# Kernel optimization log

Measured on AMD Instinct MI355X. Metric: run time of the kernel, lower is better.

Reference implementation:

```python
import jax, jax.numpy as jnp
import numpy as np

NUM_HEADS = 32
NUM_KV_HEADS = 8
HEAD_DIM = 128
SCALE = 0.08838834764831845  # 1/sqrt(HEAD_DIM)
SEQ_LEN = 2048
NEG_INF = -1e30


def setup_inputs() -> dict:
    key = jax.random.key(0)
    k1, k2, k3 = jax.random.split(key, 3)
    query = jax.random.normal(k1, (SEQ_LEN, NUM_HEADS * HEAD_DIM), dtype=jnp.float32)
    key_t = jax.random.normal(k2, (SEQ_LEN, NUM_KV_HEADS * HEAD_DIM), dtype=jnp.float32)
    value = jax.random.normal(k3, (SEQ_LEN, NUM_KV_HEADS * HEAD_DIM), dtype=jnp.float32)
    return {"query": query, "key": key_t, "value": value}


def reference(query, key, value):
    S = query.shape[0]
    n_rep = NUM_HEADS // NUM_KV_HEADS
    # GQA: group q heads by kv head instead of materializing repeated K/V.
    q = query.reshape(S, NUM_KV_HEADS, n_rep, HEAD_DIM)   # [S, G, R, D]
    k = key.reshape(S, NUM_KV_HEADS, HEAD_DIM)            # [S, G, D]
    v = value.reshape(S, NUM_KV_HEADS, HEAD_DIM)          # [S, G, D]
    # scores: [G, R, S(query), S(key)]
    scores = jnp.einsum('sgrd,tgd->grst', q, k) * jnp.float32(SCALE)
    # causal mask (prefill: seq_len > 1 -> is_causal=True)
    causal = jnp.arange(S)[:, None] >= jnp.arange(S)[None, :]  # [S, S]
    scores = jnp.where(causal, scores, NEG_INF)
    probs = jax.nn.softmax(scores, axis=-1)
    out = jnp.einsum('grst,tgd->sgrd', probs, v)          # [S, G, R, D]
    return out.reshape(S, NUM_HEADS * HEAD_DIM)
```

## Files before the change

kernel.cpp:

```cpp
#include <hip/hip_runtime.h>


#define SEQ    2048
#define NH     32
#define NKV    8
#define DHEAD  128
#define QROW   (NH * DHEAD)
#define KVROW  (NKV * DHEAD)
#define SCALE  0.08838834764831845f
#define LOG2E  1.4426950408889634f
#define BN     64
#define VSTRP  132

typedef __attribute__((ext_vector_type(8))) short bf16x8;
typedef __attribute__((ext_vector_type(8))) unsigned short u16x8;
typedef __attribute__((ext_vector_type(16))) float f32x16;
typedef __attribute__((ext_vector_type(4))) unsigned int u32x4;

static __device__ __forceinline__ unsigned short f2bf(float f) {
  unsigned int u = __float_as_uint(f);
  return (unsigned short)((u + 0x7fffu + ((u >> 16) & 1u)) >> 16);
}

static __device__ __forceinline__ unsigned cvtpk_bf16(float lo, float hi) {
  unsigned r;
  asm("v_cvt_pk_bf16_f32 %0, %1, %2" : "=v"(r) : "v"(lo), "v"(hi));
  return r;
}

static __device__ __forceinline__ f32x16 zero16() {
  f32x16 z;
#pragma unroll
  for (int i = 0; i < 16; ++i) z[i] = 0.f;
  return z;
}

__global__ __launch_bounds__(256) void prep_kernel(
    const float* __restrict__ K, const float* __restrict__ V,
    unsigned short* __restrict__ Kg, unsigned short* __restrict__ VTg) {
  __shared__ unsigned short Vs[16 * VSTRP];
  const int t0  = blockIdx.x * 16;
  const int g   = blockIdx.y;
  const int tid = threadIdx.x;
#pragma unroll
  for (int e = 0; e < 2; ++e) {
    int fi = e * 256 + tid;
    int t  = fi >> 5;
    int c4 = fi & 31;
    const float4 kv = *(const float4*)(K + (size_t)(t0 + t) * KVROW + g * DHEAD + c4 * 4);
    ushort4 kb4 = {f2bf(kv.x), f2bf(kv.y), f2bf(kv.z), f2bf(kv.w)};
    *(ushort4*)(Kg + ((size_t)(g * SEQ + t0 + t) << 7) + c4 * 4) = kb4;
    const float4 vv = *(const float4*)(V + (size_t)(t0 + t) * KVROW + g * DHEAD + c4 * 4);
    ushort4 vb4 = {f2bf(vv.x), f2bf(vv.y), f2bf(vv.z), f2bf(vv.w)};
    *(ushort4*)&Vs[t * VSTRP + c4 * 4] = vb4;
  }
  __syncthreads();
  {
    int d  = tid >> 1;
    int tb = tid & 1;
    u16x8 o;
#pragma unroll
    for (int j = 0; j < 8; ++j) o[j] = Vs[(tb * 8 + j) * VSTRP + d];
    *(u16x8*)(VTg + (size_t)(g * DHEAD + d) * SEQ + t0 + tb * 8) = o;
  }
}

static __device__ __forceinline__ void stage_tile(
    const unsigned short* __restrict__ Kg, const unsigned short* __restrict__ VTg,
    unsigned short* kbuf, unsigned short* vbuf, int g, int t, int w, int lane) {
  const int t0 = t * BN;
#pragma unroll
  for (int c = 0; c < 2; ++c) {
    int off = (w * 2 + c) * 512 + lane * 8;
    int tl  = off >> 7;
    int dsw = (off & 127) ^ (8 * (tl & 15));
    const unsigned short* src = Kg + ((size_t)(g * SEQ + t0 + tl) << 7) + dsw;
    __builtin_amdgcn_global_load_lds(
        (const __attribute__((address_space(1))) void*)src,
        (__attribute__((address_space(3))) void*)(kbuf + (w * 2 + c) * 512), 16, 0, 0);
  }
#pragma unroll
  for (int c = 0; c < 2; ++c) {
    int off = (w * 2 + c) * 512 + lane * 8;
    int dl  = off >> 6;
    int tsw = (off & 63) ^ (8 * (dl & 7));
    const unsigned short* src = VTg + (size_t)(g * DHEAD + dl) * SEQ + t0 + tsw;
    __builtin_amdgcn_global_load_lds(
        (const __attribute__((address_space(1))) void*)src,
        (__attribute__((address_space(3))) void*)(vbuf + (w * 2 + c) * 512), 16, 0, 0);
  }
}

static __device__ __forceinline__ void load_qf(
    const float* __restrict__ Q, int q0, int h, int l32, int hi, bf16x8* qf) {
  const float* qp = Q + (size_t)(q0 + l32) * QROW + h * DHEAD + hi * 8;
#pragma unroll
  for (int ks = 0; ks < 8; ++ks) {
    const float4 a = *(const float4*)(qp + ks * 16);
    const float4 c = *(const float4*)(qp + ks * 16 + 4);
    bf16x8 v;
    v[0] = (short)f2bf(a.x * (SCALE * LOG2E));
    v[1] = (short)f2bf(a.y * (SCALE * LOG2E));
    v[2] = (short)f2bf(a.z * (SCALE * LOG2E));
    v[3] = (short)f2bf(a.w * (SCALE * LOG2E));
    v[4] = (short)f2bf(c.x * (SCALE * LOG2E));
    v[5] = (short)f2bf(c.y * (SCALE * LOG2E));
    v[6] = (short)f2bf(c.z * (SCALE * LOG2E));
    v[7] = (short)f2bf(c.w * (SCALE * LOG2E));
    qf[ks] = v;
  }
}

#define PV_KSTEP(PP, S, KS2)                                                     \
  do {                                                                           \
    unsigned y0 = cvtpk_bf16((PP)[(2 * (S)) * 4 + 0], (PP)[(2 * (S)) * 4 + 1]);  \
    unsigned z0 = cvtpk_bf16((PP)[(2 * (S)) * 4 + 2], (PP)[(2 * (S)) * 4 + 3]);  \
    unsigned y1 = cvtpk_bf16((PP)[(2 * (S) + 1) * 4 + 0], (PP)[(2 * (S) + 1) * 4 + 1]); \
    unsigned z1 = cvtpk_bf16((PP)[(2 * (S) + 1) * 4 + 2], (PP)[(2 * (S) + 1) * 4 + 3]); \
    asm("v_permlane32_swap_b32 %0, %1" : "+v"(y0), "+v"(y1));                    \
    asm("v_permlane32_swap_b32 %0, %1" : "+v"(z0), "+v"(z1));                    \
    u32x4 paw = (u32x4){y0, z0, y1, z1};                                         \
    bf16x8 pa = __builtin_bit_cast(bf16x8, paw);                                 \
    const int tcol = (KS2) * 16 + hi * 8;                                        \
    _Pragma("unroll")                                                            \
    for (int nd = 0; nd < 4; ++nd) {                                             \
      int drow = nd * 32 + l32;                                                  \
      bf16x8 vf = *(const bf16x8*)&vb[drow * BN + (tcol ^ (8 * (drow & 7)))];    \
      oacc[nd] = __builtin_amdgcn_mfma_f32_32x32x16_bf16(pa, vf, oacc[nd], 0, 0, 0); \
    }                                                                            \
  } while (0)

static __device__ __forceinline__ void compute_tile(
    const unsigned short* kb, const unsigned short* vb,
    const bf16x8* qf, f32x16* oacc, float& lsum,
    int keyb, int q0, bool diag, int KB, int l32, int hi) {
  f32x16 s0 = zero16();
  f32x16 s1 = zero16();
  __builtin_amdgcn_s_setprio(1);
#pragma unroll
  for (int ks = 0; ks < 8; ++ks) {
    const int t = l32;
    bf16x8 kf = *(const bf16x8*)&kb[t * DHEAD + ((ks * 16 + hi * 8) ^ (8 * (t & 15)))];
    s0 = __builtin_amdgcn_mfma_f32_32x32x16_bf16(kf, qf[ks], s0, 0, 0, 0);
  }
  if (KB == 2) {
#pragma unroll
    for (int ks = 0; ks < 8; ++ks) {
      const int t = 32 + l32;
      bf16x8 kf = *(const bf16x8*)&kb[t * DHEAD + ((ks * 16 + hi * 8) ^ (8 * (t & 15)))];
      s1 = __builtin_amdgcn_mfma_f32_32x32x16_bf16(kf, qf[ks], s1, 0, 0, 0);
    }
  }
  __builtin_amdgcn_s_setprio(0);

  f32x16 p0, p1;
#pragma unroll
  for (int r = 0; r < 16; ++r) {
    const int ko = (r & 3) + 8 * (r >> 2) + 4 * hi;
    float x = s0[r];
    x = (diag && (keyb + ko > q0 + l32)) ? -1e30f : x;
    float e = __builtin_amdgcn_exp2f(x);
    p0[r] = e;
    lsum += e;
  }
  if (KB == 2) {
#pragma unroll
    for (int r = 0; r < 16; ++r) {
      const int ko = 32 + (r & 3) + 8 * (r >> 2) + 4 * hi;
      float x = s1[r];
      x = (diag && (keyb + ko > q0 + l32)) ? -1e30f : x;
      float e = __builtin_amdgcn_exp2f(x);
      p1[r] = e;
      lsum += e;
    }
  }

  __builtin_amdgcn_s_setprio(1);
  PV_KSTEP(p0, 0, 0);
  PV_KSTEP(p0, 1, 1);
  if (KB == 2) {
    PV_KSTEP(p1, 0, 2);
    PV_KSTEP(p1, 1, 3);
  }
  __builtin_amdgcn_s_setprio(0);
}

__global__ __launch_bounds__(512, 2) void sdpa_pair_kernel(
    const float* __restrict__ Q, float* __restrict__ O,
    const unsigned short* __restrict__ Kg, const unsigned short* __restrict__ VTg) {
  __shared__ unsigned short Kring[4][BN * DHEAD];
  __shared__ unsigned short Vring[4][DHEAD * BN];
  __shared__ float Lb[4][32];

  const int b  = blockIdx.x;
  const int g  = b & 7;
  const int p  = b >> 3;
  const int nt_l = (p + 2) >> 1;
  const int nt_h = 33 - nt_l;
  const int jj_h = 63 - p;
  const int tid  = threadIdx.x;
  const int w    = tid >> 6;
  const int lane = tid & 63;
  const int l32  = lane & 31;
  const int hi   = lane >> 5;
  const int grp  = w >> 2;
  const int wg   = w & 3;
  const int h    = g * 4 + wg;

  const int myjj_l = p;
  int q0 = (grp ? p : jj_h) * 32;

  bf16x8 qf[8];
  load_qf(Q, q0, h, l32, hi, qf);

  f32x16 oacc[4];
#pragma unroll
  for (int i = 0; i < 4; ++i) oacc[i] = zero16();
  float lsum = 0.f;

#pragma unroll
  for (int t = 0; t < 4; ++t)
    stage_tile(Kg, VTg, Kring[t], Vring[t], g, t, w, lane);
  __syncthreads();

  int ct = 0, sn = 4;
  for (int it = 0; it < 17; ++it) {
    int nc;
    if (it < nt_l) {
      const int t = it;
      const bool diag = (grp == 1) && (t == nt_l - 1);
      const int KB = (diag && !(myjj_l & 1)) ? 1 : 2;
      compute_tile(Kring[t & 3], Vring[t & 3], qf, oacc, lsum,
                   t * BN, q0, diag, KB, l32, hi);
      nc = 1;
      if (grp == 1 && t == nt_l - 1) {
        float tot = lsum + __shfl_xor(lsum, 32);
        float inv = 1.f / tot;
#pragma unroll
        for (int nd = 0; nd < 4; ++nd)
#pragma unroll
          for (int r = 0; r < 16; ++r) {
            const int row = (r & 3) + 8 * (r >> 2) + 4 * hi;
            O[(size_t)(q0 + row) * QROW + h * DHEAD + nd * 32 + l32] =
                oacc[nd][r] * __shfl(inv, row);
          }
#pragma unroll
        for (int i = 0; i < 4; ++i) oacc[i] = zero16();
        lsum = 0.f;
        q0 = jj_h * 32;
        load_qf(Q, q0, h, l32, hi, qf);
      }
    } else {
      const int j  = it - nt_l;
      const int tA = nt_l + 2 * j;
      const int t  = tA + grp;
      if (t < nt_h) {
        const bool diag = (t == nt_h - 1);
        const int KB = (diag && !(jj_h & 1)) ? 1 : 2;
        compute_tile(Kring[t & 3], Vring[t & 3], qf, oacc, lsum,
                     t * BN, q0, diag, KB, l32, hi);
      }
      nc = (tA + 1 < nt_h) ? 2 : 1;
    }
    ct += nc;
    __syncthreads();
    for (int k2 = 0; k2 < nc && sn < nt_h; ++k2, ++sn)
      stage_tile(Kg, VTg, Kring[sn & 3], Vring[sn & 3], g, sn, w, lane);
  }

  float* OvF = (float*)&Kring[0][0];
  {
    float tot = lsum + __shfl_xor(lsum, 32);
    if (grp == 1) {
      if (hi == 0) Lb[wg][l32] = tot;
      float* ob = OvF + wg * (32 * 128);
#pragma unroll
      for (int nd = 0; nd < 4; ++nd)
#pragma unroll
        for (int r = 0; r < 16; ++r) {
          const int row = (r & 3) + 8 * (r >> 2) + 4 * hi;
          ob[row * 128 + nd * 32 + l32] = oacc[nd][r];
        }
    }
    __syncthreads();
    if (grp == 0) {
      tot += Lb[wg][l32];
      float inv = 1.f / tot;
      const float* ob = OvF + wg * (32 * 128);
#pragma unroll
      for (int nd = 0; nd < 4; ++nd)
#pragma unroll
        for (int r = 0; r < 16; ++r) {
          const int row = (r & 3) + 8 * (r >> 2) + 4 * hi;
          float val = oacc[nd][r] + ob[row * 128 + nd * 32 + l32];
          O[(size_t)(q0 + row) * QROW + h * DHEAD + nd * 32 + l32] =
              val * __shfl(inv, row);
        }
    }
  }
}

extern "C" void kernel_launch(void* const* d_in, const int* in_sizes, int n_in,
                              void* d_out, int out_size, void* d_ws, size_t ws_size,
                              hipStream_t stream) {
  (void)in_sizes; (void)n_in; (void)out_size; (void)ws_size;
  const float* Q = (const float*)d_in[0];
  const float* K = (const float*)d_in[1];
  const float* V = (const float*)d_in[2];
  float* O = (float*)d_out;
  unsigned short* Kg  = (unsigned short*)d_ws;
  unsigned short* VTg = Kg + (size_t)NKV * SEQ * DHEAD;
  prep_kernel<<<dim3(SEQ / 16, NKV), 256, 0, stream>>>(K, V, Kg, VTg);
  sdpa_pair_kernel<<<256, 512, 0, stream>>>(Q, O, Kg, VTg);
}
```

Baseline: 144.0 us.

## Pre-swizzle K/V into MFMA fragment order and load fragments directly from global

The prep kernel now writes K and V as bf16 tiles already laid out in MFMA operand-fragment order. The attention kernel then reads each fragment with one coalesced 16-byte global load per lane, instead of staging tiles through an LDS ring with swizzled reads and barriers. This removes the shared-memory pipeline and per-iteration __syncthreads. It also specialises the softmax so non-diagonal tiles skip the mask test. In exchange, K/V reuse across the 8 waves now relies on L1/L2 caching instead of LDS, and nothing prefetches or overlaps the global load latency.

```diff
diff --git a/kernel.cpp b/kernel.cpp
--- a/kernel.cpp
+++ b/kernel.cpp
@@ -10,7 +10,7 @@
 #define SCALE  0.08838834764831845f
 #define LOG2E  1.4426950408889634f
 #define BN     64
-#define VSTRP  132
+#define PSTR   136
 
 typedef __attribute__((ext_vector_type(8))) short bf16x8;
 typedef __attribute__((ext_vector_type(8))) unsigned short u16x8;
@@ -35,59 +35,52 @@
   return z;
 }
 
-__global__ __launch_bounds__(256) void prep_kernel(
+__global__ __launch_bounds__(256) void prep_frag_kernel(
     const float* __restrict__ K, const float* __restrict__ V,
-    unsigned short* __restrict__ Kg, unsigned short* __restrict__ VTg) {
-  __shared__ unsigned short Vs[16 * VSTRP];
-  const int t0  = blockIdx.x * 16;
+    unsigned short* __restrict__ Kf, unsigned short* __restrict__ Vf) {
+  __shared__ unsigned short Ks[64 * PSTR];
+  __shared__ unsigned short Vs[64 * PSTR];
+  const int tb  = blockIdx.x;
   const int g   = blockIdx.y;
+  const int t0  = tb * 64;
   const int tid = threadIdx.x;
 #pragma unroll
-  for (int e = 0; e < 2; ++e) {
+  for (int e = 0; e < 8; ++e) {
     int fi = e * 256 + tid;
-    int t  = fi >> 5;
+    int r  = fi >> 5;
     int c4 = fi & 31;
-    const float4 kv = *(const float4*)(K + (size_t)(t0 + t) * KVROW + g * DHEAD + c4 * 4);
+    const float4 kv = *(const float4*)(K + (size_t)(t0 + r) * KVROW + g * DHEAD + c4 * 4);
     ushort4 kb4 = {f2bf(kv.x), f2bf(kv.y), f2bf(kv.z), f2bf(kv.w)};
-    *(ushort4*)(Kg + ((size_t)(g * SEQ + t0 + t) << 7) + c4 * 4) = kb4;
-    const float4 vv = *(const float4*)(V + (size_t)(t0 + t) * KVROW + g * DHEAD + c4 * 4);
+    *(ushort4*)&Ks[r * PSTR + c4 * 4] = kb4;
+    const float4 vv = *(const float4*)(V + (size_t)(t0 + r) * KVROW + g * DHEAD + c4 * 4);
     ushort4 vb4 = {f2bf(vv.x), f2bf(vv.y), f2bf(vv.z), f2bf(vv.w)};
-    *(ushort4*)&Vs[t * VSTRP + c4 * 4] = vb4;
+    *(ushort4*)&Vs[r * PSTR + c4 * 4] = vb4;
   }
   __syncthreads();
-  {
-    int d  = tid >> 1;
-    int tb = tid & 1;
+  const size_t tbase = ((size_t)(g * 32 + tb)) << 13;
+#pragma unroll
+  for (int q = 0; q < 4; ++q) {
+    int slot = tid * 4 + q;
+    int fk   = slot >> 6;
+    int lane = slot & 63;
+    int l32v = lane & 31, hiv = lane >> 5;
+    int row  = (fk >> 3) * 32 + l32v;
+    int col  = (fk & 7) * 16 + hiv * 8;
+    u16x8 o = *(const u16x8*)&Ks[row * PSTR + col];
+    *(u16x8*)(Kf + tbase + slot * 8) = o;
+  }
+#pragma unroll
+  for (int q = 0; q < 4; ++q) {
+    int slot = tid * 4 + q;
+    int fv   = slot >> 6;
+    int lane = slot & 63;
+    int l32v = lane & 31, hiv = lane >> 5;
+    int d    = (fv & 3) * 32 + l32v;
+    int key  = (fv >> 2) * 16 + hiv * 8;
     u16x8 o;
 #pragma unroll
-    for (int j = 0; j < 8; ++j) o[j] = Vs[(tb * 8 + j) * VSTRP + d];
-    *(u16x8*)(VTg + (size_t)(g * DHEAD + d) * SEQ + t0 + tb * 8) = o;
-  }
-}
-
-static __device__ __forceinline__ void stage_tile(
-    const unsigned short* __restrict__ Kg, const unsigned short* __restrict__ VTg,
-    unsigned short* kbuf, unsigned short* vbuf, int g, int t, int w, int lane) {
-  const int t0 = t * BN;
-#pragma unroll
-  for (int c = 0; c < 2; ++c) {
-    int off = (w * 2 + c) * 512 + lane * 8;
-    int tl  = off >> 7;
-    int dsw = (off & 127) ^ (8 * (tl & 15));
-    const unsigned short* src = Kg + ((size_t)(g * SEQ + t0 + tl) << 7) + dsw;
-    __builtin_amdgcn_global_load_lds(
-        (const __attribute__((address_space(1))) void*)src,
-        (__attribute__((address_space(3))) void*)(kbuf + (w * 2 + c) * 512), 16, 0, 0);
-  }
-#pragma unroll
-  for (int c = 0; c < 2; ++c) {
-    int off = (w * 2 + c) * 512 + lane * 8;
-    int dl  = off >> 6;
-    int tsw = (off & 63) ^ (8 * (dl & 7));
-    const unsigned short* src = VTg + (size_t)(g * DHEAD + dl) * SEQ + t0 + tsw;
-    __builtin_amdgcn_global_load_lds(
-        (const __attribute__((address_space(1))) void*)src,
-        (__attribute__((address_space(3))) void*)(vbuf + (w * 2 + c) * 512), 16, 0, 0);
+    for (int j = 0; j < 8; ++j) o[j] = Vs[(key + j) * PSTR + d];
+    *(u16x8*)(Vf + tbase + slot * 8) = o;
   }
 }
 
@@ -121,57 +114,61 @@
     asm("v_permlane32_swap_b32 %0, %1" : "+v"(z0), "+v"(z1));                    \
     u32x4 paw = (u32x4){y0, z0, y1, z1};                                         \
     bf16x8 pa = __builtin_bit_cast(bf16x8, paw);                                 \
-    const int tcol = (KS2) * 16 + hi * 8;                                        \
     _Pragma("unroll")                                                            \
     for (int nd = 0; nd < 4; ++nd) {                                             \
-      int drow = nd * 32 + l32;                                                  \
-      bf16x8 vf = *(const bf16x8*)&vb[drow * BN + (tcol ^ (8 * (drow & 7)))];    \
+      bf16x8 vf = *(const bf16x8*)(Vt + ((KS2) * 4 + nd) * 512 + lane * 8);      \
       oacc[nd] = __builtin_amdgcn_mfma_f32_32x32x16_bf16(pa, vf, oacc[nd], 0, 0, 0); \
     }                                                                            \
   } while (0)
 
-static __device__ __forceinline__ void compute_tile(
-    const unsigned short* kb, const unsigned short* vb,
+static __device__ __forceinline__ void compute_tile_g(
+    const unsigned short* __restrict__ Kt, const unsigned short* __restrict__ Vt,
     const bf16x8* qf, f32x16* oacc, float& lsum,
-    int keyb, int q0, bool diag, int KB, int l32, int hi) {
+    int keyb, int q0, bool diag, int KB, int l32, int hi, int lane) {
+  bf16x8 kf[8], kf2[8];
+#pragma unroll
+  for (int ks = 0; ks < 8; ++ks)
+    kf[ks] = *(const bf16x8*)(Kt + ks * 512 + lane * 8);
+  if (KB == 2) {
+#pragma unroll
+    for (int ks = 0; ks < 8; ++ks)
+      kf2[ks] = *(const bf16x8*)(Kt + (8 + ks) * 512 + lane * 8);
+  }
   f32x16 s0 = zero16();
   f32x16 s1 = zero16();
   __builtin_amdgcn_s_setprio(1);
 #pragma unroll
-  for (int ks = 0; ks < 8; ++ks) {
-    const int t = l32;
-    bf16x8 kf = *(const bf16x8*)&kb[t * DHEAD + ((ks * 16 + hi * 8) ^ (8 * (t & 15)))];
-    s0 = __builtin_amdgcn_mfma_f32_32x32x16_bf16(kf, qf[ks], s0, 0, 0, 0);
-  }
+  for (int ks = 0; ks < 8; ++ks)
+    s0 = __builtin_amdgcn_mfma_f32_32x32x16_bf16(kf[ks], qf[ks], s0, 0, 0, 0);
   if (KB == 2) {
 #pragma unroll
-    for (int ks = 0; ks < 8; ++ks) {
-      const int t = 32 + l32;
-      bf16x8 kf = *(const bf16x8*)&kb[t * DHEAD + ((ks * 16 + hi * 8) ^ (8 * (t & 15)))];
-      s1 = __builtin_amdgcn_mfma_f32_32x32x16_bf16(kf, qf[ks], s1, 0, 0, 0);
+    for (int ks = 0; ks < 8; ++ks)
+      s1 = __builtin_amdgcn_mfma_f32_32x32x16_bf16(kf2[ks], qf[ks], s1, 0, 0, 0);
+  }
+  __builtin_amdgcn_s_setprio(0);
+
+  f32x16 p0, p1;
+  if (!diag) {
+#pragma unroll
+    for (int r = 0; r < 16; ++r) { float e = __builtin_amdgcn_exp2f(s0[r]); p0[r] = e; lsum += e; }
+#pragma unroll
+    for (int r = 0; r < 16; ++r) { float e = __builtin_amdgcn_exp2f(s1[r]); p1[r] = e; lsum += e; }
+  } else {
+#pragma unroll
+    for (int r = 0; r < 16; ++r) {
+      const int ko = (r & 3) + 8 * (r >> 2) + 4 * hi;
+      float x = (keyb + ko > q0 + l32) ? -1e30f : s0[r];
+      float e = __builtin_amdgcn_exp2f(x);
+      p0[r] = e; lsum += e;
     }
-  }
-  __builtin_amdgcn_s_setprio(0);
-
-  f32x16 p0, p1;
-#pragma unroll
-  for (int r = 0; r < 16; ++r) {
-    const int ko = (r & 3) + 8 * (r >> 2) + 4 * hi;
-    float x = s0[r];
-    x = (diag && (keyb + ko > q0 + l32)) ? -1e30f : x;
-    float e = __builtin_amdgcn_exp2f(x);
-    p0[r] = e;
-    lsum += e;
-  }
-  if (KB == 2) {
-#pragma unroll
-    for (int r = 0; r < 16; ++r) {
-      const int ko = 32 + (r & 3) + 8 * (r >> 2) + 4 * hi;
-      float x = s1[r];
-      x = (diag && (keyb + ko > q0 + l32)) ? -1e30f : x;
-      float e = __builtin_amdgcn_exp2f(x);
-      p1[r] = e;
-      lsum += e;
+    if (KB == 2) {
+#pragma unroll
+      for (int r = 0; r < 16; ++r) {
+        const int ko = 32 + (r & 3) + 8 * (r >> 2) + 4 * hi;
+        float x = (keyb + ko > q0 + l32) ? -1e30f : s1[r];
+        float e = __builtin_amdgcn_exp2f(x);
+        p1[r] = e; lsum += e;
+      }
     }
   }
 
@@ -185,19 +182,19 @@
   __builtin_amdgcn_s_setprio(0);
 }
 
-__global__ __launch_bounds__(512, 2) void sdpa_pair_kernel(
+__global__ __launch_bounds__(512, 2) void sdpa_frag_kernel(
     const float* __restrict__ Q, float* __restrict__ O,
-    const unsigned short* __restrict__ Kg, const unsigned short* __restrict__ VTg) {
-  __shared__ unsigned short Kring[4][BN * DHEAD];
-  __shared__ unsigned short Vring[4][DHEAD * BN];
+    const unsigned short* __restrict__ Kf, const unsigned short* __restrict__ Vf) {
+  __shared__ float Obuf[4][32 * 128];
   __shared__ float Lb[4][32];
 
-  const int b  = blockIdx.x;
-  const int g  = b & 7;
-  const int p  = b >> 3;
+  const int b    = blockIdx.x;
+  const int g    = b & 7;
+  const int p    = b >> 3;
   const int nt_l = (p + 2) >> 1;
   const int nt_h = 33 - nt_l;
   const int jj_h = 63 - p;
+  const int jj_l = p;
   const int tid  = threadIdx.x;
   const int w    = tid >> 6;
   const int lane = tid & 63;
@@ -207,8 +204,7 @@
   const int wg   = w & 3;
   const int h    = g * 4 + wg;
 
-  const int myjj_l = p;
-  int q0 = (grp ? p : jj_h) * 32;
+  int q0 = (grp ? jj_l : jj_h) * 32;
 
   bf16x8 qf[8];
   load_qf(Q, q0, h, l32, hi, qf);
@@ -218,85 +214,64 @@
   for (int i = 0; i < 4; ++i) oacc[i] = zero16();
   float lsum = 0.f;
 
-#pragma unroll
-  for (int t = 0; t < 4; ++t)
-    stage_tile(Kg, VTg, Kring[t], Vring[t], g, t, w, lane);
-  __syncthreads();
-
-  int ct = 0, sn = 4;
-  for (int it = 0; it < 17; ++it) {
-    int nc;
-    if (it < nt_l) {
-      const int t = it;
-      const bool diag = (grp == 1) && (t == nt_l - 1);
-      const int KB = (diag && !(myjj_l & 1)) ? 1 : 2;
-      compute_tile(Kring[t & 3], Vring[t & 3], qf, oacc, lsum,
-                   t * BN, q0, diag, KB, l32, hi);
-      nc = 1;
-      if (grp == 1 && t == nt_l - 1) {
-        float tot = lsum + __shfl_xor(lsum, 32);
-        float inv = 1.f / tot;
-#pragma unroll
-        for (int nd = 0; nd < 4; ++nd)
-#pragma unroll
-          for (int r = 0; r < 16; ++r) {
-            const int row = (r & 3) + 8 * (r >> 2) + 4 * hi;
-            O[(size_t)(q0 + row) * QROW + h * DHEAD + nd * 32 + l32] =
-                oacc[nd][r] * __shfl(inv, row);
-          }
-#pragma unroll
-        for (int i = 0; i < 4; ++i) oacc[i] = zero16();
-        lsum = 0.f;
-        q0 = jj_h * 32;
-        load_qf(Q, q0, h, l32, hi, qf);
-      }
-    } else {
-      const int j  = it - nt_l;
-      const int tA = nt_l + 2 * j;
-      const int t  = tA + grp;
-      if (t < nt_h) {
-        const bool diag = (t == nt_h - 1);
-        const int KB = (diag && !(jj_h & 1)) ? 1 : 2;
-        compute_tile(Kring[t & 3], Vring[t & 3], qf, oacc, lsum,
-                     t * BN, q0, diag, KB, l32, hi);
-      }
-      nc = (tA + 1 < nt_h) ? 2 : 1;
-    }
-    ct += nc;
-    __syncthreads();
-    for (int k2 = 0; k2 < nc && sn < nt_h; ++k2, ++sn)
-      stage_tile(Kg, VTg, Kring[sn & 3], Vring[sn & 3], g, sn, w, lane);
-  }
-
-  float* OvF = (float*)&Kring[0][0];
-  {
-    float tot = lsum + __shfl_xor(lsum, 32);
-    if (grp == 1) {
-      if (hi == 0) Lb[wg][l32] = tot;
-      float* ob = OvF + wg * (32 * 128);
+  const int niters = grp ? 16 : 17;
+#pragma unroll 1
+  for (int i = 0; i < niters; ++i) {
+    int t, jjc;
+    bool diag;
+    if (grp == 0)      { t = i;                jjc = jj_h; diag = (nt_h == 17) && (i == 16); }
+    else if (i < nt_l) { t = i;                jjc = jj_l; diag = (i == nt_l - 1); }
+    else               { t = 17 + i - nt_l;    jjc = jj_h; diag = (i == 15); }
+    const int KB = (diag && !(jjc & 1)) ? 1 : 2;
+    const unsigned short* Kt = Kf + (((size_t)(g * 32 + t)) << 13);
+    const unsigned short* Vt = Vf + (((size_t)(g * 32 + t)) << 13);
+    compute_tile_g(Kt, Vt, qf, oacc, lsum, t * BN, q0, diag, KB, l32, hi, lane);
+
+    if (grp == 1 && i == nt_l - 1) {
+      float tot = lsum + __shfl_xor(lsum, 32);
+      float inv = 1.f / tot;
 #pragma unroll
       for (int nd = 0; nd < 4; ++nd)
 #pragma unroll
         for (int r = 0; r < 16; ++r) {
           const int row = (r & 3) + 8 * (r >> 2) + 4 * hi;
-          ob[row * 128 + nd * 32 + l32] = oacc[nd][r];
+          O[(size_t)(q0 + row) * QROW + h * DHEAD + nd * 32 + l32] =
+              oacc[nd][r] * __shfl(inv, row);
         }
+#pragma unroll
+      for (int i2 = 0; i2 < 4; ++i2) oacc[i2] = zero16();
+      lsum = 0.f;
+      q0 = jj_h * 32;
+      load_qf(Q, q0, h, l32, hi, qf);
     }
-    __syncthreads();
-    if (grp == 0) {
-      tot += Lb[wg][l32];
-      float inv = 1.f / tot;
-      const float* ob = OvF + wg * (32 * 128);
-#pragma unroll
-      for (int nd = 0; nd < 4; ++nd)
-#pragma unroll
-        for (int r = 0; r < 16; ++r) {
-          const int row = (r & 3) + 8 * (r >> 2) + 4 * hi;
-          float val = oacc[nd][r] + ob[row * 128 + nd * 32 + l32];
-          O[(size_t)(q0 + row) * QROW + h * DHEAD + nd * 32 + l32] =
-              val * __shfl(inv, row);
-        }
-    }
+  }
+
+  float tot = lsum + __shfl_xor(lsum, 32);
+  if (grp == 1) {
+    if (hi == 0) Lb[wg][l32] = tot;
+    float* ob = &Obuf[wg][0];
+#pragma unroll
+    for (int nd = 0; nd < 4; ++nd)
+#pragma unroll
+      for (int r = 0; r < 16; ++r) {
+        const int row = (r & 3) + 8 * (r >> 2) + 4 * hi;
+        ob[row * 128 + nd * 32 + l32] = oacc[nd][r];
+      }
+  }
+  __syncthreads();
+  if (grp == 0) {
+    tot += Lb[wg][l32];
+    float inv = 1.f / tot;
+    const float* ob = &Obuf[wg][0];
+#pragma unroll
+    for (int nd = 0; nd < 4; ++nd)
+#pragma unroll
+      for (int r = 0; r < 16; ++r) {
+        const int row = (r & 3) + 8 * (r >> 2) + 4 * hi;
+        float val = oacc[nd][r] + ob[row * 128 + nd * 32 + l32];
+        O[(size_t)(q0 + row) * QROW + h * DHEAD + nd * 32 + l32] =
+            val * __shfl(inv, row);
+      }
   }
 }
 
@@ -308,8 +283,8 @@
   const float* K = (const float*)d_in[1];
   const float* V = (const float*)d_in[2];
   float* O = (float*)d_out;
-  unsigned short* Kg  = (unsigned short*)d_ws;
-  unsigned short* VTg = Kg + (size_t)NKV * SEQ * DHEAD;
-  prep_kernel<<<dim3(SEQ / 16, NKV), 256, 0, stream>>>(K, V, Kg, VTg);
-  sdpa_pair_kernel<<<256, 512, 0, stream>>>(Q, O, Kg, VTg);
-}
+  unsigned short* Kf = (unsigned short*)d_ws;
+  unsigned short* Vf = Kf + (size_t)NKV * SEQ * DHEAD;
+  prep_frag_kernel<<<dim3(32, 8), 256, 0, stream>>>(K, V, Kf, Vf);
+  sdpa_frag_kernel<<<256, 512, 0, stream>>>(Q, O, Kf, Vf);
+}
```

After: 152.6 us. +6.0%, slower.
